# Optimization experiments

Hardware: AMD Instinct MI355X
Metric: run time of the kernel (lower is better)

Reference implementation:

```python
import jax, jax.numpy as jnp
import numpy as np
import itertools

B, N, K, G = 1024, 1024, 6, 720  # G = K!
H1, H2, C = 64, 32, 40
IN = K * 3


def setup_inputs() -> dict:
    key = jax.random.key(0)
    ks = jax.random.split(key, 8)
    x = jax.random.normal(ks[0], (B, N, 3), dtype=jnp.float32)
    # per-sample subsample indices (torch uses randperm(N)[:K]; distinctness
    # is irrelevant to the math, randint keeps them in-range)
    idx = jax.random.randint(ks[1], (B, K), 0, N)
    perms = jnp.asarray(
        np.array(list(itertools.permutations(range(K))), dtype=np.int32)
    )  # (G, K)
    # MLP params: torch Linear default init ~ U(-1/sqrt(fan_in), 1/sqrt(fan_in))
    def lin(k, fin, fout):
        kw, kb = jax.random.split(k)
        s = 1.0 / np.sqrt(fin)
        W = jax.random.uniform(kw, (fin, fout), jnp.float32, -s, s)
        b = jax.random.uniform(kb, (fout,), jnp.float32, -s, s)
        return W, b
    W1, b1 = lin(ks[2], IN, H1)
    W2, b2 = lin(ks[3], H1, H2)
    W3, b3 = lin(ks[4], H2, C)
    return dict(x=x, W1=W1, b1=b1, W2=W2, b2=b2, W3=W3, b3=b3,
                idx=idx, perms=perms)


def reference(x, W1, b1, W2, b2, W3, b3, idx, perms):
    Bv = x.shape[0]
    Gv, Kv = perms.shape
    # gather the K subsampled points per batch element: (B, K, 3)
    pts = jnp.take_along_axis(x, idx[:, :, None], axis=1)
    # expand over all K! permutations of the point ordering: (B, G, K, 3)
    permuted = pts[:, perms, :]
    flat = permuted.reshape(Bv, Gv, Kv * 3)  # (B, G, K*3)
    h = jax.nn.relu(flat @ W1 + b1)          # (B, G, H1)
    h = jax.nn.relu(h @ W2 + b2)             # (B, G, H2)
    y = h @ W3 + b3                          # (B, G, C)
    return y.mean(axis=1)                    # (B, C)
```

## Files before the change

kernel.cpp:

```cpp
#include <hip/hip_runtime.h>
#include <hip/hip_bf16.h>

typedef __attribute__((ext_vector_type(8))) short short8;
typedef __attribute__((ext_vector_type(4))) float f32x4;
typedef __attribute__((ext_vector_type(4))) unsigned int u32x4;
typedef __attribute__((ext_vector_type(2))) unsigned int u32x2;

#define NN 1024

#define LFENCE { asm volatile("s_waitcnt lgkmcnt(0)" ::: "memory"); __builtin_amdgcn_sched_barrier(0); }

#define ROW_W(ROW, VAL) { \
  float v_ = fmaxf((VAL), 0.0f); \
  __hip_bfloat16 hb_ = __float2bfloat16(v_); \
  wb[((ROW) * 64) + (lane ^ ((((ROW)) & 7) << 3))] = *(short*)&hb_; \
}

#define ROW6(R, BX) \
  ROW_W((R)+0,(BX)+T0_) ROW_W((R)+1,(BX)+T1_) ROW_W((R)+2,(BX)+T2_) \
  ROW_W((R)+3,(BX)+T3_) ROW_W((R)+4,(BX)+T4_) ROW_W((R)+5,(BX)+T5_)

#define SGR(A0,A1,A2, M0,M1,M2) do { \
  const float f0_ = b1v + P[(A0)*6+0]; \
  const float f1_ = b1v + P[(A1)*6+0]; \
  const float f2_ = b1v + P[(A2)*6+0]; \
  const float g12_ = P[(A1)*6+1] + P[(A2)*6+2]; \
  const float g21_ = P[(A2)*6+1] + P[(A1)*6+2]; \
  const float g02_ = P[(A0)*6+1] + P[(A2)*6+2]; \
  const float g20_ = P[(A2)*6+1] + P[(A0)*6+2]; \
  const float g01_ = P[(A0)*6+1] + P[(A1)*6+2]; \
  const float g10_ = P[(A1)*6+1] + P[(A0)*6+2]; \
  const float e0_ = P[(M0)*6+3], e1_ = P[(M1)*6+3], e2_ = P[(M2)*6+3]; \
  const float h12_ = P[(M1)*6+4] + P[(M2)*6+5]; \
  const float h21_ = P[(M2)*6+4] + P[(M1)*6+5]; \
  const float h02_ = P[(M0)*6+4] + P[(M2)*6+5]; \
  const float h20_ = P[(M2)*6+4] + P[(M0)*6+5]; \
  const float h01_ = P[(M0)*6+4] + P[(M1)*6+5]; \
  const float h10_ = P[(M1)*6+4] + P[(M0)*6+5]; \
  const float T0_ = e0_+h12_, T1_ = e0_+h21_, T2_ = e1_+h02_; \
  const float T3_ = e1_+h20_, T4_ = e2_+h01_, T5_ = e2_+h10_; \
  const float B0_ = f0_+g12_, B1_ = f0_+g21_, B2_ = f1_+g02_; \
  const float B3_ = f1_+g20_, B4_ = f2_+g01_, B5_ = f2_+g10_; \
  ROW6(0,  B0_) ROW6(6,  B1_) ROW6(12, B2_) \
  ROW6(18, B3_) ROW6(24, B4_) ROW6(30, B5_) \
} while(0)

#define MFMA8(A0_, A1_) do { \
  f32x4 c0_ = {b2v0,b2v0,b2v0,b2v0}; \
  f32x4 c1_ = {b2v1,b2v1,b2v1,b2v1}; \
  c0_ = __builtin_amdgcn_mfma_f32_16x16x32_bf16(A0_, bh00, c0_, 0,0,0); \
  c0_ = __builtin_amdgcn_mfma_f32_16x16x32_bf16(A1_, bh10, c0_, 0,0,0); \
  c0_ = __builtin_amdgcn_mfma_f32_16x16x32_bf16(A0_, bl00, c0_, 0,0,0); \
  c0_ = __builtin_amdgcn_mfma_f32_16x16x32_bf16(A1_, bl10, c0_, 0,0,0); \
  c1_ = __builtin_amdgcn_mfma_f32_16x16x32_bf16(A0_, bh01, c1_, 0,0,0); \
  c1_ = __builtin_amdgcn_mfma_f32_16x16x32_bf16(A1_, bh11, c1_, 0,0,0); \
  c1_ = __builtin_amdgcn_mfma_f32_16x16x32_bf16(A0_, bl01, c1_, 0,0,0); \
  c1_ = __builtin_amdgcn_mfma_f32_16x16x32_bf16(A1_, bl11, c1_, 0,0,0); \
  acc0[0]+=fmaxf(c0_[0],0.f); acc0[1]+=fmaxf(c0_[1],0.f); \
  acc0[2]+=fmaxf(c0_[2],0.f); acc0[3]+=fmaxf(c0_[3],0.f); \
  acc1[0]+=fmaxf(c1_[0],0.f); acc1[1]+=fmaxf(c1_[1],0.f); \
  acc1[2]+=fmaxf(c1_[2],0.f); acc1[3]+=fmaxf(c1_[3],0.f); \
} while(0)

#define PHASEB3 do { \
  LFENCE; \
  _Pragma("unroll") \
  for (int t_ = 0; t_ < 3; ++t_) { \
    short8 A0_ = *(const short8*)&wb[t_ * 1024 + e0i]; \
    short8 A1_ = *(const short8*)&wb[t_ * 1024 + e1i]; \
    MFMA8(A0_, A1_); \
  } \
} while(0)

#define CH1(A0,A1,A2, M0,M1,M2) do { SGR(A0,A1,A2, M0,M1,M2); PHASEB3; } while(0)

#define MKB(dst_h, dst_l, KH, NIDX) do { \
  _Pragma("unroll") \
  for (int e_ = 0; e_ < 8; ++e_) { \
    float f_ = W2[((KH)*32 + kg*8 + e_)*32 + 16*(NIDX) + colb]; \
    __hip_bfloat16 hi_ = __float2bfloat16(f_); \
    float lof_ = f_ - __bfloat162float(hi_); \
    __hip_bfloat16 lo_ = __float2bfloat16(lof_); \
    dst_h[e_] = *(short*)&hi_; dst_l[e_] = *(short*)&lo_; \
  } \
} while(0)

__global__ __launch_bounds__(256, 2) void symm_mlp_kernel(
    const float* __restrict__ x,
    const float* __restrict__ W1, const float* __restrict__ b1,
    const float* __restrict__ W2, const float* __restrict__ b2,
    const float* __restrict__ W3, const float* __restrict__ b3,
    const int* __restrict__ idx, const int* __restrict__ perms,
    float* __restrict__ out)
{
    __shared__ short h1s[4][48 * 64];
    __shared__ float redbuf[4][32];

    const int tid   = threadIdx.x;
    const int lane  = tid & 63;
    const int wv    = tid >> 6;
    const int batch = blockIdx.x;

    float P[36];
    {
        float w1c[18];
        #pragma unroll
        for (int r = 0; r < 18; ++r) w1c[r] = W1[r * 64 + lane];

        float px[6][3];
        #pragma unroll
        for (int k = 0; k < 6; ++k) {
            int p = idx[batch * 6 + k];
            #pragma unroll
            for (int d = 0; d < 3; ++d) px[k][d] = x[(batch * NN + p) * 3 + d];
        }
        #pragma unroll
        for (int k = 0; k < 6; ++k)
        #pragma unroll
        for (int j = 0; j < 6; ++j)
            P[k*6+j] = fmaf(px[k][2], w1c[3*j+2], fmaf(px[k][1], w1c[3*j+1], px[k][0] * w1c[3*j+0]));
    }
    const float b1v = b1[lane];

    const int colb = lane & 15, kg = lane >> 4;
    short8 bh00, bl00, bh10, bl10, bh01, bl01, bh11, bl11;
    MKB(bh00, bl00, 0, 0);
    MKB(bh10, bl10, 1, 0);
    MKB(bh01, bl01, 0, 1);
    MKB(bh11, bl11, 1, 1);
    const float b2v0 = b2[colb];
    const float b2v1 = b2[16 + colb];

    short* wb = &h1s[wv][0];
    *reinterpret_cast<u32x4*>(&wb[2304 + lane * 8]) = u32x4{0u, 0u, 0u, 0u};
    *reinterpret_cast<u32x2*>(&wb[2816 + lane * 4]) = u32x2{0u, 0u};

    const int Xl  = (lane & 7) << 3;
    const int e0i = (lane & 15) * 64 + ((kg * 8) ^ Xl);
    const int e1i = (lane & 15) * 64 + ((32 + kg * 8) ^ Xl);

    f32x4 acc0 = {0.f,0.f,0.f,0.f}, acc1 = {0.f,0.f,0.f,0.f};

    if (wv == 0) {
        CH1(0,1,2, 3,4,5);  CH1(0,1,3, 2,4,5);  CH1(0,1,4, 2,3,5);
        CH1(0,1,5, 2,3,4);  CH1(0,2,3, 1,4,5);
    } else if (wv == 1) {
        CH1(0,2,4, 1,3,5);  CH1(0,2,5, 1,3,4);  CH1(0,3,4, 1,2,5);
        CH1(0,3,5, 1,2,4);  CH1(0,4,5, 1,2,3);
    } else if (wv == 2) {
        CH1(1,2,3, 0,4,5);  CH1(1,2,4, 0,3,5);  CH1(1,2,5, 0,3,4);
        CH1(1,3,4, 0,2,5);  CH1(1,3,5, 0,2,4);
    } else {
        CH1(1,4,5, 0,2,3);  CH1(2,3,4, 0,1,5);  CH1(2,3,5, 0,1,4);
        CH1(2,4,5, 0,1,3);  CH1(3,4,5, 0,1,2);
    }

    float s0 = acc0[0] + acc0[1] + acc0[2] + acc0[3];
    float s1 = acc1[0] + acc1[1] + acc1[2] + acc1[3];
    s0 += __shfl_xor(s0, 16, 64);  s0 += __shfl_xor(s0, 32, 64);
    s1 += __shfl_xor(s1, 16, 64);  s1 += __shfl_xor(s1, 32, 64);
    s0 -= 60.0f * fmaxf(b2v0, 0.0f);
    s1 -= 60.0f * fmaxf(b2v1, 0.0f);

    if (lane < 16)       redbuf[wv][lane]      = s0;
    else if (lane < 32)  redbuf[wv][lane]      = s1;
    __syncthreads();

    if (tid < 40) {
        float m[32];
        #pragma unroll
        for (int c = 0; c < 32; ++c)
            m[c] = (redbuf[0][c] + redbuf[1][c] + redbuf[2][c] + redbuf[3][c]) * (1.0f / 720.0f);
        float y = b3[tid];
        #pragma unroll
        for (int c = 0; c < 32; ++c) y = fmaf(m[c], W3[c * 40 + tid], y);
        out[batch * 40 + tid] = y;
    }
}

extern "C" void kernel_launch(void* const* d_in, const int* in_sizes, int n_in,
                              void* d_out, int out_size, void* d_ws, size_t ws_size,
                              hipStream_t stream) {
    const float* x  = (const float*)d_in[0];
    const float* W1 = (const float*)d_in[1];
    const float* b1 = (const float*)d_in[2];
    const float* W2 = (const float*)d_in[3];
    const float* b2 = (const float*)d_in[4];
    const float* W3 = (const float*)d_in[5];
    const float* b3 = (const float*)d_in[6];
    const int* idx   = (const int*)d_in[7];
    const int* perms = (const int*)d_in[8];
    (void)perms;
    float* out = (float*)d_out;

    symm_mlp_kernel<<<1024, 256, 0, stream>>>(x, W1, b1, W2, b2, W3, b3, idx, perms, out);
}
```

Baseline: 21.36 us.

## Drop bf16 hi/lo split for W2 and double-buffer h1 tiles in LDS

Removes the low-part bf16 correction MFMAs for W2, halving the layer-2 matrix work, and stops computing and holding the lo fragments. It adds a second per-wave LDS buffer so the h1 rows for the next chunk are written and read while the MFMAs for the previous chunk run. It also reorders the prologue loads so the idx and x gather is issued first. Using only single bf16 weights lowers layer-2 accuracy, and the extra LDS buffer and live read registers may cut occupancy.

Result: faster. 20.09 us (-5.9%).

```diff
diff --git a/kernel.cpp b/kernel.cpp
--- a/kernel.cpp
+++ b/kernel.cpp
@@ -10,17 +10,17 @@
 
 #define LFENCE { asm volatile("s_waitcnt lgkmcnt(0)" ::: "memory"); __builtin_amdgcn_sched_barrier(0); }
 
-#define ROW_W(ROW, VAL) { \
+#define ROW_W(BUF, ROW, VAL) { \
   float v_ = fmaxf((VAL), 0.0f); \
   __hip_bfloat16 hb_ = __float2bfloat16(v_); \
-  wb[((ROW) * 64) + (lane ^ ((((ROW)) & 7) << 3))] = *(short*)&hb_; \
+  BUF[((ROW) * 64) + (lane ^ ((((ROW)) & 7) << 3))] = *(short*)&hb_; \
 }
 
-#define ROW6(R, BX) \
-  ROW_W((R)+0,(BX)+T0_) ROW_W((R)+1,(BX)+T1_) ROW_W((R)+2,(BX)+T2_) \
-  ROW_W((R)+3,(BX)+T3_) ROW_W((R)+4,(BX)+T4_) ROW_W((R)+5,(BX)+T5_)
-
-#define SGR(A0,A1,A2, M0,M1,M2) do { \
+#define ROW6(BUF, R, BX) \
+  ROW_W(BUF,(R)+0,(BX)+T0_) ROW_W(BUF,(R)+1,(BX)+T1_) ROW_W(BUF,(R)+2,(BX)+T2_) \
+  ROW_W(BUF,(R)+3,(BX)+T3_) ROW_W(BUF,(R)+4,(BX)+T4_) ROW_W(BUF,(R)+5,(BX)+T5_)
+
+#define SGR(BUF, A0,A1,A2, M0,M1,M2) do { \
   const float f0_ = b1v + P[(A0)*6+0]; \
   const float f1_ = b1v + P[(A1)*6+0]; \
   const float f2_ = b1v + P[(A2)*6+0]; \
@@ -41,47 +41,38 @@
   const float T3_ = e1_+h20_, T4_ = e2_+h01_, T5_ = e2_+h10_; \
   const float B0_ = f0_+g12_, B1_ = f0_+g21_, B2_ = f1_+g02_; \
   const float B3_ = f1_+g20_, B4_ = f2_+g01_, B5_ = f2_+g10_; \
-  ROW6(0,  B0_) ROW6(6,  B1_) ROW6(12, B2_) \
-  ROW6(18, B3_) ROW6(24, B4_) ROW6(30, B5_) \
+  ROW6(BUF, 0,  B0_) ROW6(BUF, 6,  B1_) ROW6(BUF, 12, B2_) \
+  ROW6(BUF, 18, B3_) ROW6(BUF, 24, B4_) ROW6(BUF, 30, B5_) \
 } while(0)
 
-#define MFMA8(A0_, A1_) do { \
+#define MFMA4T(A0_, A1_) do { \
   f32x4 c0_ = {b2v0,b2v0,b2v0,b2v0}; \
   f32x4 c1_ = {b2v1,b2v1,b2v1,b2v1}; \
   c0_ = __builtin_amdgcn_mfma_f32_16x16x32_bf16(A0_, bh00, c0_, 0,0,0); \
   c0_ = __builtin_amdgcn_mfma_f32_16x16x32_bf16(A1_, bh10, c0_, 0,0,0); \
-  c0_ = __builtin_amdgcn_mfma_f32_16x16x32_bf16(A0_, bl00, c0_, 0,0,0); \
-  c0_ = __builtin_amdgcn_mfma_f32_16x16x32_bf16(A1_, bl10, c0_, 0,0,0); \
   c1_ = __builtin_amdgcn_mfma_f32_16x16x32_bf16(A0_, bh01, c1_, 0,0,0); \
   c1_ = __builtin_amdgcn_mfma_f32_16x16x32_bf16(A1_, bh11, c1_, 0,0,0); \
-  c1_ = __builtin_amdgcn_mfma_f32_16x16x32_bf16(A0_, bl01, c1_, 0,0,0); \
-  c1_ = __builtin_amdgcn_mfma_f32_16x16x32_bf16(A1_, bl11, c1_, 0,0,0); \
   acc0[0]+=fmaxf(c0_[0],0.f); acc0[1]+=fmaxf(c0_[1],0.f); \
   acc0[2]+=fmaxf(c0_[2],0.f); acc0[3]+=fmaxf(c0_[3],0.f); \
   acc1[0]+=fmaxf(c1_[0],0.f); acc1[1]+=fmaxf(c1_[1],0.f); \
   acc1[2]+=fmaxf(c1_[2],0.f); acc1[3]+=fmaxf(c1_[3],0.f); \
 } while(0)
 
-#define PHASEB3 do { \
-  LFENCE; \
-  _Pragma("unroll") \
-  for (int t_ = 0; t_ < 3; ++t_) { \
-    short8 A0_ = *(const short8*)&wb[t_ * 1024 + e0i]; \
-    short8 A1_ = *(const short8*)&wb[t_ * 1024 + e1i]; \
-    MFMA8(A0_, A1_); \
-  } \
-} while(0)
-
-#define CH1(A0,A1,A2, M0,M1,M2) do { SGR(A0,A1,A2, M0,M1,M2); PHASEB3; } while(0)
-
-#define MKB(dst_h, dst_l, KH, NIDX) do { \
+#define READS(BUF) { \
+  r0 = *(const short8*)&BUF[0*1024 + e0i]; r1 = *(const short8*)&BUF[0*1024 + e1i]; \
+  r2 = *(const short8*)&BUF[1*1024 + e0i]; r3 = *(const short8*)&BUF[1*1024 + e1i]; \
+  r4 = *(const short8*)&BUF[2*1024 + e0i]; r5 = *(const short8*)&BUF[2*1024 + e1i]; }
+
+#define MFMA3 { MFMA4T(r0,r1); MFMA4T(r2,r3); MFMA4T(r4,r5); }
+
+#define CHUNK(BUF, A0,A1,A2, M0,M1,M2) { SGR(BUF, A0,A1,A2, M0,M1,M2); READS(BUF); LFENCE; }
+
+#define MKB(dst_h, KH, NIDX) do { \
   _Pragma("unroll") \
   for (int e_ = 0; e_ < 8; ++e_) { \
     float f_ = W2[((KH)*32 + kg*8 + e_)*32 + 16*(NIDX) + colb]; \
     __hip_bfloat16 hi_ = __float2bfloat16(f_); \
-    float lof_ = f_ - __bfloat162float(hi_); \
-    __hip_bfloat16 lo_ = __float2bfloat16(lof_); \
-    dst_h[e_] = *(short*)&hi_; dst_l[e_] = *(short*)&lo_; \
+    dst_h[e_] = *(short*)&hi_; \
   } \
 } while(0)
 
@@ -90,10 +81,10 @@
     const float* __restrict__ W1, const float* __restrict__ b1,
     const float* __restrict__ W2, const float* __restrict__ b2,
     const float* __restrict__ W3, const float* __restrict__ b3,
-    const int* __restrict__ idx, const int* __restrict__ perms,
+    const int* __restrict__ idx,
     float* __restrict__ out)
 {
-    __shared__ short h1s[4][48 * 64];
+    __shared__ short h1s[4][2][48 * 64];
     __shared__ float redbuf[4][32];
 
     const int tid   = threadIdx.x;
@@ -101,58 +92,80 @@
     const int wv    = tid >> 6;
     const int batch = blockIdx.x;
 
-    float P[36];
-    {
-        float w1c[18];
+    int pidx[6];
+    #pragma unroll
+    for (int k = 0; k < 6; ++k) pidx[k] = idx[batch * 6 + k];
+
+    float px[6][3];
+    #pragma unroll
+    for (int k = 0; k < 6; ++k)
         #pragma unroll
-        for (int r = 0; r < 18; ++r) w1c[r] = W1[r * 64 + lane];
-
-        float px[6][3];
-        #pragma unroll
-        for (int k = 0; k < 6; ++k) {
-            int p = idx[batch * 6 + k];
-            #pragma unroll
-            for (int d = 0; d < 3; ++d) px[k][d] = x[(batch * NN + p) * 3 + d];
-        }
-        #pragma unroll
-        for (int k = 0; k < 6; ++k)
-        #pragma unroll
-        for (int j = 0; j < 6; ++j)
-            P[k*6+j] = fmaf(px[k][2], w1c[3*j+2], fmaf(px[k][1], w1c[3*j+1], px[k][0] * w1c[3*j+0]));
-    }
+        for (int d = 0; d < 3; ++d) px[k][d] = x[(batch * NN + pidx[k]) * 3 + d];
+
+    float w1c[18];
+    #pragma unroll
+    for (int r = 0; r < 18; ++r) w1c[r] = W1[r * 64 + lane];
+
     const float b1v = b1[lane];
-
     const int colb = lane & 15, kg = lane >> 4;
-    short8 bh00, bl00, bh10, bl10, bh01, bl01, bh11, bl11;
-    MKB(bh00, bl00, 0, 0);
-    MKB(bh10, bl10, 1, 0);
-    MKB(bh01, bl01, 0, 1);
-    MKB(bh11, bl11, 1, 1);
     const float b2v0 = b2[colb];
     const float b2v1 = b2[16 + colb];
 
-    short* wb = &h1s[wv][0];
-    *reinterpret_cast<u32x4*>(&wb[2304 + lane * 8]) = u32x4{0u, 0u, 0u, 0u};
-    *reinterpret_cast<u32x2*>(&wb[2816 + lane * 4]) = u32x2{0u, 0u};
+    short8 bh00, bh10, bh01, bh11;
+    MKB(bh00, 0, 0);
+    MKB(bh10, 1, 0);
+    MKB(bh01, 0, 1);
+    MKB(bh11, 1, 1);
+
+    float P[36];
+    #pragma unroll
+    for (int k = 0; k < 6; ++k)
+    #pragma unroll
+    for (int j = 0; j < 6; ++j)
+        P[k*6+j] = fmaf(px[k][2], w1c[3*j+2], fmaf(px[k][1], w1c[3*j+1], px[k][0] * w1c[3*j+0]));
+
+    short* wb0 = &h1s[wv][0][0];
+    short* wb1 = &h1s[wv][1][0];
+    *reinterpret_cast<u32x4*>(&wb0[2304 + lane * 8]) = u32x4{0u,0u,0u,0u};
+    *reinterpret_cast<u32x2*>(&wb0[2816 + lane * 4]) = u32x2{0u,0u};
+    *reinterpret_cast<u32x4*>(&wb1[2304 + lane * 8]) = u32x4{0u,0u,0u,0u};
+    *reinterpret_cast<u32x2*>(&wb1[2816 + lane * 4]) = u32x2{0u,0u};
 
     const int Xl  = (lane & 7) << 3;
     const int e0i = (lane & 15) * 64 + ((kg * 8) ^ Xl);
     const int e1i = (lane & 15) * 64 + ((32 + kg * 8) ^ Xl);
 
     f32x4 acc0 = {0.f,0.f,0.f,0.f}, acc1 = {0.f,0.f,0.f,0.f};
+    short8 r0, r1, r2, r3, r4, r5;
 
     if (wv == 0) {
-        CH1(0,1,2, 3,4,5);  CH1(0,1,3, 2,4,5);  CH1(0,1,4, 2,3,5);
-        CH1(0,1,5, 2,3,4);  CH1(0,2,3, 1,4,5);
+        CHUNK(wb0, 0,1,2, 3,4,5);
+        MFMA3; CHUNK(wb1, 0,1,3, 2,4,5);
+        MFMA3; CHUNK(wb0, 0,1,4, 2,3,5);
+        MFMA3; CHUNK(wb1, 0,1,5, 2,3,4);
+        MFMA3; CHUNK(wb0, 0,2,3, 1,4,5);
+        MFMA3;
     } else if (wv == 1) {
-        CH1(0,2,4, 1,3,5);  CH1(0,2,5, 1,3,4);  CH1(0,3,4, 1,2,5);
-        CH1(0,3,5, 1,2,4);  CH1(0,4,5, 1,2,3);
+        CHUNK(wb0, 0,2,4, 1,3,5);
+        MFMA3; CHUNK(wb1, 0,2,5, 1,3,4);
+        MFMA3; CHUNK(wb0, 0,3,4, 1,2,5);
+        MFMA3; CHUNK(wb1, 0,3,5, 1,2,4);
+        MFMA3; CHUNK(wb0, 0,4,5, 1,2,3);
+        MFMA3;
     } else if (wv == 2) {
-        CH1(1,2,3, 0,4,5);  CH1(1,2,4, 0,3,5);  CH1(1,2,5, 0,3,4);
-        CH1(1,3,4, 0,2,5);  CH1(1,3,5, 0,2,4);
+        CHUNK(wb0, 1,2,3, 0,4,5);
+        MFMA3; CHUNK(wb1, 1,2,4, 0,3,5);
+        MFMA3; CHUNK(wb0, 1,2,5, 0,3,4);
+        MFMA3; CHUNK(wb1, 1,3,4, 0,2,5);
+        MFMA3; CHUNK(wb0, 1,3,5, 0,2,4);
+        MFMA3;
     } else {
-        CH1(1,4,5, 0,2,3);  CH1(2,3,4, 0,1,5);  CH1(2,3,5, 0,1,4);
-        CH1(2,4,5, 0,1,3);  CH1(3,4,5, 0,1,2);
+        CHUNK(wb0, 1,4,5, 0,2,3);
+        MFMA3; CHUNK(wb1, 2,3,4, 0,1,5);
+        MFMA3; CHUNK(wb0, 2,3,5, 0,1,4);
+        MFMA3; CHUNK(wb1, 2,4,5, 0,1,3);
+        MFMA3; CHUNK(wb0, 3,4,5, 0,1,2);
+        MFMA3;
     }
 
     float s0 = acc0[0] + acc0[1] + acc0[2] + acc0[3];
@@ -162,8 +175,8 @@
     s0 -= 60.0f * fmaxf(b2v0, 0.0f);
     s1 -= 60.0f * fmaxf(b2v1, 0.0f);
 
-    if (lane < 16)       redbuf[wv][lane]      = s0;
-    else if (lane < 32)  redbuf[wv][lane]      = s1;
+    if (lane < 16)       redbuf[wv][lane] = s0;
+    else if (lane < 32)  redbuf[wv][lane] = s1;
     __syncthreads();
 
     if (tid < 40) {
@@ -189,9 +202,7 @@
     const float* W3 = (const float*)d_in[5];
     const float* b3 = (const float*)d_in[6];
     const int* idx   = (const int*)d_in[7];
-    const int* perms = (const int*)d_in[8];
-    (void)perms;
     float* out = (float*)d_out;
 
-    symm_mlp_kernel<<<1024, 256, 0, stream>>>(x, W1, b1, W2, b2, W3, b3, idx, perms, out);
+    symm_mlp_kernel<<<1024, 256, 0, stream>>>(x, W1, b1, W2, b2, W3, b3, idx, out);
 }
```
